# Optimization experiments

Hardware: AMD Instinct MI355X
Metric: run time of the kernel (lower is better)

The kernel has to match this reference:

```python
import jax, jax.numpy as jnp
import numpy as np


def _mw_weight(m):
    if m == 1:
        return 1j * np.pi / 2
    if m == -1:
        return -1j * np.pi / 2
    if m % 2 == 0:
        return 2.0 / (1 - m * m)
    return 0.0


def quad_weights_mw(L):
    # Exact MW quadrature weights (McEwen & Wiaux 2011), folded to L theta samples.
    ms = np.arange(-(L - 1), L)
    w = np.array([_mw_weight(m) for m in ms], dtype=np.complex128)
    w *= np.exp(-1j * ms * np.pi / (2 * L - 1))
    wr = np.real(np.fft.fft(np.fft.ifftshift(w))) / (2 * L - 1)
    q = wr[:L].copy()
    q[: L - 1] += wr[2 * L - 2 : L - 1 : -1]  # fold extended-grid weights (spin=0)
    return q * 2 * np.pi / (2 * L - 1)


def legendre_table(L, theta):
    # Normalized assoc. Legendre Pbar_{lm}(cos theta) incl. sqrt((2l+1)/4pi (l-m)!/(l+m)!)
    # and Condon-Shortley phase. Returns (L, 2L-1, ntheta) with m index = m + L - 1.
    ct, st = np.cos(theta), np.sin(theta)
    nt = theta.shape[0]
    P = np.zeros((L, L, nt))
    P[0, 0] = 1.0 / np.sqrt(4 * np.pi)
    for m in range(1, L):
        P[m, m] = -np.sqrt((2 * m + 1) / (2.0 * m)) * st * P[m - 1, m - 1]
    for m in range(0, L - 1):
        P[m + 1, m] = np.sqrt(2 * m + 3.0) * ct * P[m, m]
    for m in range(0, L):
        for l in range(m + 2, L):
            a = np.sqrt((4.0 * l * l - 1) / (l * l - m * m))
            b = np.sqrt(((2.0 * l + 1) * ((l - 1) ** 2 - m * m)) / ((2.0 * l - 3) * (l * l - m * m)))
            P[l, m] = a * ct * P[l - 1, m] - b * P[l - 2, m]
    full = np.zeros((L, 2 * L - 1, nt))
    for m in range(0, L):
        full[:, L - 1 + m] = P[:, m]
        if m > 0:
            full[:, L - 1 - m] = ((-1) ** m) * P[:, m]
    return full


def _mw_theta(L):
    return np.pi * (2 * np.arange(L) + 1) / (2 * L - 1)


def sht_forward(f, L, plm, weights):
    # f: (L, 2L-1, C) real -> flm: (L, 2L-1, C) complex
    nphi = 2 * L - 1
    ms = np.arange(-(L - 1), L)
    Fm = jnp.fft.fft(f, axis=1)[:, ms % nphi, :]  # (ntheta, 2L-1, C)
    return jnp.einsum('t,lmt,tmc->lmc', weights, plm, Fm)


def sht_inverse(flm, L, plm):
    # flm: (L, 2L-1, C) complex -> real field (L, 2L-1, C)
    nphi = 2 * L - 1
    ms = np.arange(-(L - 1), L)
    G = jnp.einsum('lmc,lmt->tmc', flm, plm)  # (ntheta, 2L-1, C)
    Gfull = jnp.zeros_like(G).at[:, ms % nphi, :].set(G)
    return jnp.real(jnp.fft.ifft(Gfull, axis=1) * nphi)


def resize_flm(flm, L_new):
    L_old = flm.shape[0]
    if L_new == L_old:
        return flm
    if L_new < L_old:
        return flm[:L_new, L_old - L_new : L_old + L_new - 1]
    out = jnp.zeros((L_new, 2 * L_new - 1) + flm.shape[2:], flm.dtype)
    return out.at[:L_old, L_new - L_old : L_new + L_old - 1].set(flm)


def setup_inputs() -> dict:
    key = jax.random.key(0)
    ks = jax.random.split(key, 6)
    L_in, Lf, L_out = 128, 64, 128
    Cin, Cout, T = 64, 64, 256
    return {
        'x': jax.random.normal(ks[0], (L_in, 2 * L_in - 1, Cin), jnp.float32),
        't_emb': jax.random.normal(ks[1], (T,), jnp.float32),
        'A_real': 0.01 * jax.random.normal(ks[2], (Lf, 2 * Lf - 1, T), jnp.float32),
        'A_imag': 0.01 * jax.random.normal(ks[3], (Lf, 2 * Lf - 1, T), jnp.float32),
        'R_real': 0.01 * jax.random.normal(ks[4], (Lf, 2 * Lf - 1, Cout, Cin), jnp.float32),
        'R_imag': 0.01 * jax.random.normal(ks[5], (Lf, 2 * Lf - 1, Cout, Cin), jnp.float32),
        'L_out_spatial': L_out,
    }


def reference(x, t_emb, A_real, A_imag, R_real, R_imag, L_out_spatial):
    L_in = x.shape[0]
    Lf = A_real.shape[0]
    plm_in = jnp.asarray(legendre_table(L_in, _mw_theta(L_in)), jnp.float32)
    w_in = jnp.asarray(quad_weights_mw(L_in), jnp.float32)
    flm = sht_forward(x, L_in, plm_in, w_in)            # (L_in, 2L_in-1, Cin)
    flm = resize_flm(flm, Lf)                           # (Lf, 2Lf-1, Cin)
    t_c = (jnp.einsum('t,lmt->lm', t_emb, A_real)
           + 1j * jnp.einsum('t,lmt->lm', t_emb, A_imag))
    R = R_real + 1j * R_imag                            # (Lf, 2Lf-1, O, I)
    Rt = jnp.einsum('lm,lmoi->loi', t_c, R)
    flm_out = jnp.einsum('lmi,loi->lmo', flm, Rt)
    flm_out = resize_flm(flm_out, L_out_spatial)
    plm_out = jnp.asarray(legendre_table(L_out_spatial, _mw_theta(L_out_spatial)), jnp.float32)
    return sht_inverse(flm_out, L_out_spatial, plm_out)  # (L_out, 2L_out-1, O)
```

## Files before the change

### kernel.cpp

```cpp
#include <hip/hip_runtime.h>
#include <math.h>

#define PI_D 3.14159265358979323846
static const size_t OFF_P   = 0;
static const size_t OFF_W   = 524288;
static const size_t OFF_TW  = 524416;
static const size_t OFF_FMW = 524928;
static const size_t OFF_TC  = 1573504;
static const size_t OFF_FLM = 1589760;
static const size_t OFF_RT  = 2114048;
static const size_t OFF_FO  = 2638336;
static const size_t OFF_G   = 524928;
static const size_t WS_FLOATS = 3678720;

__global__ __launch_bounds__(256) void k_tables(float* __restrict__ w, float2* __restrict__ tw) {
  int t = blockIdx.x;
  int tid = threadIdx.x;
  if (t == 0 && tid < 255) {
    double a = 2.0 * PI_D * tid / 255.0;
    tw[tid] = make_float2((float)cos(a), (float)sin(a));
  }
  double term = 0.0;
  if (tid < 255) {
    int m = tid - 127;
    double br = 0.0, bi = 0.0; bool active = true;
    if (m == 1) bi = PI_D / 2.0;
    else if (m == -1) bi = -PI_D / 2.0;
    else if ((m & 1) == 0) br = 2.0 / (1.0 - (double)m * (double)m);
    else active = false;
    if (active) {
      double md = (double)m;
      double ca = cos(PI_D * md / 255.0), sa = -sin(PI_D * md / 255.0);
      double wr = br * ca - bi * sa;
      double wi = br * sa + bi * ca;
      double a1 = 2.0 * PI_D * md * t / 255.0;
      double fr = cos(a1), fi = -sin(a1);
      if (t < 127) {
        double a2 = 2.0 * PI_D * md * (t + 1) / 255.0;
        fr += cos(a2); fi += sin(a2);
      }
      term = wr * fr - wi * fi;
    }
  }
  __shared__ double red[256];
  red[tid] = term;
  __syncthreads();
  for (int off = 128; off; off >>= 1) {
    if (tid < off) red[tid] += red[tid + off];
    __syncthreads();
  }
  if (tid == 0) w[t] = (float)(red[0] * 2.0 * PI_D / (255.0 * 255.0));
}

__global__ __launch_bounds__(128) void k_legendre(float* __restrict__ P) {
  int m = blockIdx.x, t = threadIdx.x;
  double th = PI_D * (2 * t + 1) / 255.0;
  double ct = cos(th), st = sin(th);
  double pmm = 0.28209479177387814;
  for (int k = 1; k <= m; ++k) pmm *= -sqrt((2.0 * k + 1.0) / (2.0 * k)) * st;
  float* Pm = P + ((size_t)m * 64) * 128;
  Pm[(size_t)m * 128 + t] = (float)pmm;
  if (m + 1 < 64) {
    double p0 = pmm, p1 = sqrt(2.0 * m + 3.0) * ct * pmm;
    Pm[(size_t)(m + 1) * 128 + t] = (float)p1;
    for (int l = m + 2; l < 64; ++l) {
      double ll = (double)l * l, mm = (double)m * m;
      double a = sqrt((4.0 * ll - 1.0) / (ll - mm));
      double b = sqrt((2.0 * l + 1.0) * ((double)(l - 1) * (l - 1) - mm) / ((2.0 * l - 3.0) * (ll - mm)));
      double pl = a * ct * p1 - b * p0;
      Pm[(size_t)l * 128 + t] = (float)pl;
      p0 = p1; p1 = pl;
    }
  }
}

__global__ __launch_bounds__(256) void k_fwd_dft(const float* __restrict__ x, const float* __restrict__ w,
                                                 const float2* __restrict__ tw, float2* __restrict__ Fmw) {
  int t = blockIdx.x, mq = blockIdx.y;
  __shared__ float xs[255 * 64];
  int tid = threadIdx.x;
  for (int idx = tid; idx < 255 * 64; idx += 256) xs[idx] = x[(size_t)t * (255 * 64) + idx];
  __syncthreads();
  int c = tid & 63, ms = tid >> 6;
  int m0 = mq * 8 + ms * 2;
  float2 wm0 = tw[m0], wm1 = tw[m0 + 1];
  float cr0 = wm0.x, ci0 = -wm0.y;
  float cr1 = wm1.x, ci1 = -wm1.y;
  float tr0 = 1.f, ti0 = 0.f, tr1 = 1.f, ti1 = 0.f;
  float a0r = 0.f, a0i = 0.f, a1r = 0.f, a1i = 0.f;
#pragma unroll 5
  for (int p = 0; p < 255; ++p) {
    float xv = xs[p * 64 + c];
    a0r += xv * tr0; a0i += xv * ti0;
    a1r += xv * tr1; a1i += xv * ti1;
    float n0 = tr0 * cr0 - ti0 * ci0; ti0 = tr0 * ci0 + ti0 * cr0; tr0 = n0;
    float n1 = tr1 * cr1 - ti1 * ci1; ti1 = tr1 * ci1 + ti1 * cr1; tr1 = n1;
  }
  float wt = w[t];
  Fmw[((size_t)m0 * 128 + t) * 64 + c] = make_float2(wt * a0r, wt * a0i);
  Fmw[((size_t)(m0 + 1) * 128 + t) * 64 + c] = make_float2(wt * a1r, wt * a1i);
}

__global__ __launch_bounds__(256) void k_tc(const float* __restrict__ te, const float* __restrict__ Ar,
                                            const float* __restrict__ Ai, float2* __restrict__ tc) {
  int bid = blockIdx.x;
  int tid = threadIdx.x;
  float e = te[tid];
  float vr = Ar[(size_t)bid * 256 + tid] * e;
  float vi = Ai[(size_t)bid * 256 + tid] * e;
  for (int off = 32; off; off >>= 1) {
    vr += __shfl_down(vr, off);
    vi += __shfl_down(vi, off);
  }
  __shared__ float2 red[4];
  if ((tid & 63) == 0) red[tid >> 6] = make_float2(vr, vi);
  __syncthreads();
  if (tid == 0) {
    float2 s = red[0];
    for (int q = 1; q < 4; ++q) { s.x += red[q].x; s.y += red[q].y; }
    tc[bid] = s;
  }
}

__global__ __launch_bounds__(256) void k_rt(const float* __restrict__ Rr, const float* __restrict__ Ri,
                                            const float2* __restrict__ tc, float2* __restrict__ Rt) {
  int l = blockIdx.x, og = blockIdx.y;
  int tid = threadIdx.x;
  __shared__ float2 tcs[127];
  if (tid < 127) tcs[tid] = tc[l * 127 + tid];
  __syncthreads();
  int slot = tid & 63;
  int jq = tid >> 6;
  int ic = slot & 15, ol = slot >> 4;
  int o = og * 4 + ol;
  const float* rr = Rr + ((size_t)l * 127) * 4096 + o * 64 + ic * 4;
  const float* ri = Ri + ((size_t)l * 127) * 4096 + o * 64 + ic * 4;
  float4 ar = make_float4(0.f, 0.f, 0.f, 0.f);
  float4 ai = make_float4(0.f, 0.f, 0.f, 0.f);
#pragma unroll 4
  for (int j = jq; j < 127; j += 4) {
    float2 w2 = tcs[j];
    float4 a = *reinterpret_cast<const float4*>(rr + (size_t)j * 4096);
    float4 b = *reinterpret_cast<const float4*>(ri + (size_t)j * 4096);
    ar.x += w2.x * a.x - w2.y * b.x;  ai.x += w2.x * b.x + w2.y * a.x;
    ar.y += w2.x * a.y - w2.y * b.y;  ai.y += w2.x * b.y + w2.y * a.y;
    ar.z += w2.x * a.z - w2.y * b.z;  ai.z += w2.x * b.z + w2.y * a.z;
    ar.w += w2.x * a.w - w2.y * b.w;  ai.w += w2.x * b.w + w2.y * a.w;
  }
  __shared__ float4 redr[256];
  __shared__ float4 redi[256];
  redr[tid] = ar; redi[tid] = ai;
  __syncthreads();
  if (jq == 0) {
#pragma unroll
    for (int q = 1; q < 4; ++q) {
      float4 a = redr[q * 64 + slot];
      float4 b = redi[q * 64 + slot];
      ar.x += a.x; ar.y += a.y; ar.z += a.z; ar.w += a.w;
      ai.x += b.x; ai.y += b.y; ai.z += b.z; ai.w += b.w;
    }
    float4* rt4 = reinterpret_cast<float4*>(Rt);
    size_t base = ((size_t)l * 64 + o) * 32 + ic * 2;
    rt4[base]     = make_float4(ar.x, ai.x, ar.y, ai.y);
    rt4[base + 1] = make_float4(ar.z, ai.z, ar.w, ai.w);
  }
}

__global__ __launch_bounds__(256) void k_flm(const float* __restrict__ P, const float2* __restrict__ Fmw,
                                             float2* __restrict__ flm) {
  int m = blockIdx.x, lq = blockIdx.y;
  int tid = threadIdx.x;
  int c = tid & 63, lg = tid >> 6;
  __shared__ float2 Fs[32][64];
  __shared__ float Ps[8][32];
  float2 acc[2];
  acc[0] = make_float2(0.f, 0.f);
  acc[1] = make_float2(0.f, 0.f);
  for (int q = 0; q < 4; ++q) {
    __syncthreads();
    for (int idx = tid; idx < 2048; idx += 256) {
      int tt = idx >> 6, cc = idx & 63;
      Fs[tt][cc] = Fmw[((size_t)m * 128 + q * 32 + tt) * 64 + cc];
    }
    {
      int ll = tid >> 5, tt2 = tid & 31;
      int l = m + lq * 8 + ll;
      Ps[ll][tt2] = (l < 64) ? P[((size_t)m * 64 + l) * 128 + q * 32 + tt2] : 0.f;
    }
    __syncthreads();
    int li = lg * 2;
#pragma unroll 8
    for (int tt = 0; tt < 32; ++tt) {
      float2 f = Fs[tt][c];
      float p0 = Ps[li][tt], p1 = Ps[li + 1][tt];
      acc[0].x += p0 * f.x; acc[0].y += p0 * f.y;
      acc[1].x += p1 * f.x; acc[1].y += p1 * f.y;
    }
  }
#pragma unroll
  for (int s = 0; s < 2; ++s) {
    int l = m + lq * 8 + lg * 2 + s;
    if (l < 64) flm[((size_t)l * 64 + m) * 64 + c] = acc[s];
  }
}

__global__ __launch_bounds__(256) void k_flmout(const float2* __restrict__ flm, const float2* __restrict__ Rt,
                                                float2* __restrict__ fo) {
  int l = blockIdx.x, jg = blockIdx.y;
  int o = threadIdx.x & 63, js = threadIdx.x >> 6;
  __shared__ float2 Rts[64][65];
  __shared__ float2 Fjs[16][64];
  for (int idx = threadIdx.x; idx < 4096; idx += 256) {
    int oo = idx >> 6, ii = idx & 63;
    Rts[oo][ii] = Rt[((size_t)l * 64 + oo) * 64 + ii];
  }
  for (int idx = threadIdx.x; idx < 1024; idx += 256) {
    int jl = idx >> 6, ii = idx & 63;
    int j = jg * 16 + jl;
    float2 v = make_float2(0.f, 0.f);
    if (j < 127) {
      int mm = j - 63, am = mm < 0 ? -mm : mm;
      if (l >= am) {
        float2 f = flm[((size_t)l * 64 + am) * 64 + ii];
        if (mm < 0) { float s = (am & 1) ? -1.f : 1.f; v = make_float2(s * f.x, -s * f.y); }
        else v = f;
      }
    }
    Fjs[jl][ii] = v;
  }
  __syncthreads();
  float2 acc[4];
#pragma unroll
  for (int q = 0; q < 4; ++q) acc[q] = make_float2(0.f, 0.f);
  for (int i = 0; i < 64; ++i) {
    float2 r = Rts[o][i];
#pragma unroll
    for (int q = 0; q < 4; ++q) {
      float2 f = Fjs[js * 4 + q][i];
      acc[q].x += f.x * r.x - f.y * r.y;
      acc[q].y += f.x * r.y + f.y * r.x;
    }
  }
#pragma unroll
  for (int q = 0; q < 4; ++q) {
    int j = jg * 16 + js * 4 + q;
    if (j < 127) fo[((size_t)l * 127 + j) * 64 + o] = acc[q];
  }
}

__global__ __launch_bounds__(256) void k_g(const float* __restrict__ P, const float2* __restrict__ fo,
                                           float2* __restrict__ G) {
  int j = blockIdx.x, tg = blockIdx.y;
  int mm = j - 63, am = mm < 0 ? -mm : mm;
  float sgn = (mm < 0 && (am & 1)) ? -1.f : 1.f;
  int o = threadIdx.x & 63, ts = threadIdx.x >> 6;
  __shared__ float Ps[64][64];
  __shared__ float2 Fos[64][64];
  for (int idx = threadIdx.x; idx < 4096; idx += 256) {
    int ll = idx >> 6, tt = idx & 63;
    Ps[ll][tt] = P[((size_t)am * 64 + ll) * 128 + tg * 64 + tt];
  }
  for (int idx = threadIdx.x; idx < 4096; idx += 256) {
    int ll = idx >> 6, oo = idx & 63;
    float2 v = fo[((size_t)ll * 127 + j) * 64 + oo];
    Fos[ll][oo] = make_float2(sgn * v.x, sgn * v.y);
  }
  __syncthreads();
  float ar[16], ai2[16];
#pragma unroll
  for (int r = 0; r < 16; ++r) { ar[r] = 0.f; ai2[r] = 0.f; }
  for (int l = am; l < 64; ++l) {
    float2 f = Fos[l][o];
#pragma unroll
    for (int q = 0; q < 4; ++q) {
      float4 pv = *reinterpret_cast<const float4*>(&Ps[l][ts * 16 + q * 4]);
      ar[q * 4 + 0] += pv.x * f.x;  ai2[q * 4 + 0] += pv.x * f.y;
      ar[q * 4 + 1] += pv.y * f.x;  ai2[q * 4 + 1] += pv.y * f.y;
      ar[q * 4 + 2] += pv.z * f.x;  ai2[q * 4 + 2] += pv.z * f.y;
      ar[q * 4 + 3] += pv.w * f.x;  ai2[q * 4 + 3] += pv.w * f.y;
    }
  }
#pragma unroll
  for (int r = 0; r < 16; ++r) {
    int t = tg * 64 + ts * 16 + r;
    G[((size_t)t * 127 + j) * 64 + o] = make_float2(ar[r], ai2[r]);
  }
}

__global__ __launch_bounds__(256) void k_idft(const float2* __restrict__ G, const float2* __restrict__ tw,
                                              float* __restrict__ out) {
  int t = blockIdx.x, pq = blockIdx.y;
  int pl = threadIdx.x & 63, og = threadIdx.x >> 6;
  __shared__ __align__(16) unsigned char smem[65536];
  float2 (*CSs)[64] = reinterpret_cast<float2(*)[64]>(smem);
  float (*Ls)[65] = reinterpret_cast<float(*)[65]>(smem);
  for (int idx = threadIdx.x; idx < 4096; idx += 256) {
    int m = idx >> 6, oo = idx & 63;
    float2 v;
    if (m == 0) {
      float2 g = G[((size_t)t * 127 + 63) * 64 + oo];
      v = make_float2(g.x, 0.f);
    } else {
      float2 gp = G[((size_t)t * 127 + 63 + m) * 64 + oo];
      float2 gm = G[((size_t)t * 127 + 63 - m) * 64 + oo];
      v = make_float2(gp.x + gm.x, gm.y - gp.y);
    }
    CSs[m][oo] = v;
  }
  __syncthreads();
  int p = pq * 64 + pl;
  float2 wp = tw[p < 255 ? p : 0];
  float twr = 1.f, twi = 0.f;
  float acc[16];
#pragma unroll
  for (int r = 0; r < 16; ++r) acc[r] = 0.f;
  int ob = og * 16;
  for (int m = 0; m < 64; ++m) {
#pragma unroll
    for (int q = 0; q < 8; ++q) {
      float4 cs = *reinterpret_cast<const float4*>(&CSs[m][ob + q * 2]);
      acc[q * 2 + 0] += cs.x * twr + cs.y * twi;
      acc[q * 2 + 1] += cs.z * twr + cs.w * twi;
    }
    float nr = twr * wp.x - twi * wp.y;
    twi = twr * wp.y + twi * wp.x;
    twr = nr;
  }
  __syncthreads();
#pragma unroll
  for (int r = 0; r < 16; ++r) Ls[pl][ob + r] = acc[r];
  __syncthreads();
  for (int idx = threadIdx.x; idx < 4096; idx += 256) {
    int rr = idx >> 6, oo = idx & 63;
    int pg = pq * 64 + rr;
    if (pg < 255) out[((size_t)t * 255 + pg) * 64 + oo] = Ls[rr][oo];
  }
}

extern "C" void kernel_launch(void* const* d_in, const int* in_sizes, int n_in,
                              void* d_out, int out_size, void* d_ws, size_t ws_size,
                              hipStream_t stream) {
  (void)in_sizes; (void)n_in; (void)out_size;
  if (ws_size < WS_FLOATS * sizeof(float)) return;

  const float* x  = (const float*)d_in[0];
  const float* te = (const float*)d_in[1];
  const float* Ar = (const float*)d_in[2];
  const float* Ai = (const float*)d_in[3];
  const float* Rr = (const float*)d_in[4];
  const float* Ri = (const float*)d_in[5];
  float* out = (float*)d_out;

  float* ws = (float*)d_ws;
  float*  P   = ws + OFF_P;
  float*  w   = ws + OFF_W;
  float2* tw  = (float2*)(ws + OFF_TW);
  float2* Fmw = (float2*)(ws + OFF_FMW);
  float2* tc  = (float2*)(ws + OFF_TC);
  float2* flm = (float2*)(ws + OFF_FLM);
  float2* Rt  = (float2*)(ws + OFF_RT);
  float2* fo  = (float2*)(ws + OFF_FO);
  float2* G   = (float2*)(ws + OFF_G);

  k_tables<<<128, 256, 0, stream>>>(w, tw);
  k_legendre<<<64, 128, 0, stream>>>(P);
  k_fwd_dft<<<dim3(128, 8), 256, 0, stream>>>(x, w, tw, Fmw);
  k_tc<<<64 * 127, 256, 0, stream>>>(te, Ar, Ai, tc);
  k_rt<<<dim3(64, 16), 256, 0, stream>>>(Rr, Ri, tc, Rt);
  k_flm<<<dim3(64, 8), 256, 0, stream>>>(P, Fmw, flm);
  k_flmout<<<dim3(64, 8), 256, 0, stream>>>(flm, Rt, fo);
  k_g<<<dim3(127, 2), 256, 0, stream>>>(P, fo, G);
  k_idft<<<dim3(128, 4), 256, 0, stream>>>(G, tw, out);
}
```

Before: 420.7 us.

## Fuse forward DFT and Rt contraction into one interleaved kernel with chunked staging

New measurement: 390.8 us. 1.08x faster.

```diff
diff --git a/kernel.cpp b/kernel.cpp
--- a/kernel.cpp
+++ b/kernel.cpp
@@ -74,33 +74,6 @@
   }
 }
 
-__global__ __launch_bounds__(256) void k_fwd_dft(const float* __restrict__ x, const float* __restrict__ w,
-                                                 const float2* __restrict__ tw, float2* __restrict__ Fmw) {
-  int t = blockIdx.x, mq = blockIdx.y;
-  __shared__ float xs[255 * 64];
-  int tid = threadIdx.x;
-  for (int idx = tid; idx < 255 * 64; idx += 256) xs[idx] = x[(size_t)t * (255 * 64) + idx];
-  __syncthreads();
-  int c = tid & 63, ms = tid >> 6;
-  int m0 = mq * 8 + ms * 2;
-  float2 wm0 = tw[m0], wm1 = tw[m0 + 1];
-  float cr0 = wm0.x, ci0 = -wm0.y;
-  float cr1 = wm1.x, ci1 = -wm1.y;
-  float tr0 = 1.f, ti0 = 0.f, tr1 = 1.f, ti1 = 0.f;
-  float a0r = 0.f, a0i = 0.f, a1r = 0.f, a1i = 0.f;
-#pragma unroll 5
-  for (int p = 0; p < 255; ++p) {
-    float xv = xs[p * 64 + c];
-    a0r += xv * tr0; a0i += xv * ti0;
-    a1r += xv * tr1; a1i += xv * ti1;
-    float n0 = tr0 * cr0 - ti0 * ci0; ti0 = tr0 * ci0 + ti0 * cr0; tr0 = n0;
-    float n1 = tr1 * cr1 - ti1 * ci1; ti1 = tr1 * ci1 + ti1 * cr1; tr1 = n1;
-  }
-  float wt = w[t];
-  Fmw[((size_t)m0 * 128 + t) * 64 + c] = make_float2(wt * a0r, wt * a0i);
-  Fmw[((size_t)(m0 + 1) * 128 + t) * 64 + c] = make_float2(wt * a1r, wt * a1i);
-}
-
 __global__ __launch_bounds__(256) void k_tc(const float* __restrict__ te, const float* __restrict__ Ar,
                                             const float* __restrict__ Ai, float2* __restrict__ tc) {
   int bid = blockIdx.x;
@@ -122,47 +95,89 @@
   }
 }
 
-__global__ __launch_bounds__(256) void k_rt(const float* __restrict__ Rr, const float* __restrict__ Ri,
-                                            const float2* __restrict__ tc, float2* __restrict__ Rt) {
-  int l = blockIdx.x, og = blockIdx.y;
+__global__ __launch_bounds__(256) void k_fused(const float* __restrict__ x, const float* __restrict__ w,
+                                               const float2* __restrict__ tw, float2* __restrict__ Fmw,
+                                               const float* __restrict__ Rr, const float* __restrict__ Ri,
+                                               const float2* __restrict__ tc, float2* __restrict__ Rt) {
+  __shared__ union SM {
+    float xs[64 * 64];
+    struct {
+      float2 tcs[127];
+      float4 redr[256];
+      float4 redi[256];
+    } rt;
+  } sm;
+  int bid = blockIdx.x;
   int tid = threadIdx.x;
-  __shared__ float2 tcs[127];
-  if (tid < 127) tcs[tid] = tc[l * 127 + tid];
-  __syncthreads();
-  int slot = tid & 63;
-  int jq = tid >> 6;
-  int ic = slot & 15, ol = slot >> 4;
-  int o = og * 4 + ol;
-  const float* rr = Rr + ((size_t)l * 127) * 4096 + o * 64 + ic * 4;
-  const float* ri = Ri + ((size_t)l * 127) * 4096 + o * 64 + ic * 4;
-  float4 ar = make_float4(0.f, 0.f, 0.f, 0.f);
-  float4 ai = make_float4(0.f, 0.f, 0.f, 0.f);
+  int id = bid >> 1;
+
+  if ((bid & 1) == 0) {
+    int t = id >> 3, mq = id & 7;
+    int c = tid & 63, ms = tid >> 6;
+    int m0 = mq * 8 + ms * 2;
+    float2 wm0 = tw[m0], wm1 = tw[m0 + 1];
+    float cr0 = wm0.x, ci0 = -wm0.y;
+    float cr1 = wm1.x, ci1 = -wm1.y;
+    float tr0 = 1.f, ti0 = 0.f, tr1 = 1.f, ti1 = 0.f;
+    float a0r = 0.f, a0i = 0.f, a1r = 0.f, a1i = 0.f;
+    const float* xrow = x + (size_t)t * (255 * 64);
+    for (int ch = 0; ch < 4; ++ch) {
+      int plen = (ch == 3) ? 63 : 64;
+      __syncthreads();
+      const float4* src = reinterpret_cast<const float4*>(xrow + ch * 64 * 64);
+      int n4 = plen * 16;
+      for (int idx = tid; idx < n4; idx += 256)
+        reinterpret_cast<float4*>(sm.xs)[idx] = src[idx];
+      __syncthreads();
 #pragma unroll 4
-  for (int j = jq; j < 127; j += 4) {
-    float2 w2 = tcs[j];
-    float4 a = *reinterpret_cast<const float4*>(rr + (size_t)j * 4096);
-    float4 b = *reinterpret_cast<const float4*>(ri + (size_t)j * 4096);
-    ar.x += w2.x * a.x - w2.y * b.x;  ai.x += w2.x * b.x + w2.y * a.x;
-    ar.y += w2.x * a.y - w2.y * b.y;  ai.y += w2.x * b.y + w2.y * a.y;
-    ar.z += w2.x * a.z - w2.y * b.z;  ai.z += w2.x * b.z + w2.y * a.z;
-    ar.w += w2.x * a.w - w2.y * b.w;  ai.w += w2.x * b.w + w2.y * a.w;
-  }
-  __shared__ float4 redr[256];
-  __shared__ float4 redi[256];
-  redr[tid] = ar; redi[tid] = ai;
-  __syncthreads();
-  if (jq == 0) {
-#pragma unroll
-    for (int q = 1; q < 4; ++q) {
-      float4 a = redr[q * 64 + slot];
-      float4 b = redi[q * 64 + slot];
-      ar.x += a.x; ar.y += a.y; ar.z += a.z; ar.w += a.w;
-      ai.x += b.x; ai.y += b.y; ai.z += b.z; ai.w += b.w;
-    }
-    float4* rt4 = reinterpret_cast<float4*>(Rt);
-    size_t base = ((size_t)l * 64 + o) * 32 + ic * 2;
-    rt4[base]     = make_float4(ar.x, ai.x, ar.y, ai.y);
-    rt4[base + 1] = make_float4(ar.z, ai.z, ar.w, ai.w);
+      for (int p = 0; p < plen; ++p) {
+        float xv = sm.xs[p * 64 + c];
+        a0r += xv * tr0; a0i += xv * ti0;
+        a1r += xv * tr1; a1i += xv * ti1;
+        float n0 = tr0 * cr0 - ti0 * ci0; ti0 = tr0 * ci0 + ti0 * cr0; tr0 = n0;
+        float n1 = tr1 * cr1 - ti1 * ci1; ti1 = tr1 * ci1 + ti1 * cr1; tr1 = n1;
+      }
+    }
+    float wt = w[t];
+    Fmw[((size_t)m0 * 128 + t) * 64 + c] = make_float2(wt * a0r, wt * a0i);
+    Fmw[((size_t)(m0 + 1) * 128 + t) * 64 + c] = make_float2(wt * a1r, wt * a1i);
+  } else {
+    int l = id >> 4, og = id & 15;
+    if (tid < 127) sm.rt.tcs[tid] = tc[l * 127 + tid];
+    __syncthreads();
+    int slot = tid & 63;
+    int jq = tid >> 6;
+    int ic = slot & 15, ol = slot >> 4;
+    int o = og * 4 + ol;
+    const float* rr = Rr + ((size_t)l * 127) * 4096 + o * 64 + ic * 4;
+    const float* ri = Ri + ((size_t)l * 127) * 4096 + o * 64 + ic * 4;
+    float4 ar = make_float4(0.f, 0.f, 0.f, 0.f);
+    float4 ai = make_float4(0.f, 0.f, 0.f, 0.f);
+#pragma unroll 4
+    for (int j = jq; j < 127; j += 4) {
+      float2 w2 = sm.rt.tcs[j];
+      float4 a = *reinterpret_cast<const float4*>(rr + (size_t)j * 4096);
+      float4 b = *reinterpret_cast<const float4*>(ri + (size_t)j * 4096);
+      ar.x += w2.x * a.x - w2.y * b.x;  ai.x += w2.x * b.x + w2.y * a.x;
+      ar.y += w2.x * a.y - w2.y * b.y;  ai.y += w2.x * b.y + w2.y * a.y;
+      ar.z += w2.x * a.z - w2.y * b.z;  ai.z += w2.x * b.z + w2.y * a.z;
+      ar.w += w2.x * a.w - w2.y * b.w;  ai.w += w2.x * b.w + w2.y * a.w;
+    }
+    sm.rt.redr[tid] = ar; sm.rt.redi[tid] = ai;
+    __syncthreads();
+    if (jq == 0) {
+#pragma unroll
+      for (int q = 1; q < 4; ++q) {
+        float4 a = sm.rt.redr[q * 64 + slot];
+        float4 b = sm.rt.redi[q * 64 + slot];
+        ar.x += a.x; ar.y += a.y; ar.z += a.z; ar.w += a.w;
+        ai.x += b.x; ai.y += b.y; ai.z += b.z; ai.w += b.w;
+      }
+      float4* rt4 = reinterpret_cast<float4*>(Rt);
+      size_t base = ((size_t)l * 64 + o) * 32 + ic * 2;
+      rt4[base]     = make_float4(ar.x, ai.x, ar.y, ai.y);
+      rt4[base + 1] = make_float4(ar.z, ai.z, ar.w, ai.w);
+    }
   }
 }
 
@@ -364,9 +379,8 @@
 
   k_tables<<<128, 256, 0, stream>>>(w, tw);
   k_legendre<<<64, 128, 0, stream>>>(P);
-  k_fwd_dft<<<dim3(128, 8), 256, 0, stream>>>(x, w, tw, Fmw);
   k_tc<<<64 * 127, 256, 0, stream>>>(te, Ar, Ai, tc);
-  k_rt<<<dim3(64, 16), 256, 0, stream>>>(Rr, Ri, tc, Rt);
+  k_fused<<<2048, 256, 0, stream>>>(x, w, tw, Fmw, Rr, Ri, tc, Rt);
   k_flm<<<dim3(64, 8), 256, 0, stream>>>(P, Fmw, flm);
   k_flmout<<<dim3(64, 8), 256, 0, stream>>>(flm, Rt, fo);
   k_g<<<dim3(127, 2), 256, 0, stream>>>(P, fo, G);
```
